# Kernel optimization log

Measured on AMD Instinct MI355X. Metric: run time of the kernel, lower is better.

## Reference

```python
import jax, jax.numpy as jnp
import numpy as np

B, S, D, E = 4, 2048, 1024, 8
HD = D // E          # per-expert head dim = 128
ROPE = HD // 2       # rotary dims = 64 (32 complex pairs)


def setup_inputs() -> dict:
    key = jax.random.key(0)
    ks = jax.random.split(key, 5)
    x = jax.random.normal(ks[0], (B, S, D), dtype=jnp.float32)
    Wg = jax.random.normal(ks[1], (D, E), dtype=jnp.float32) * 0.02
    Wqkv = jax.random.normal(ks[2], (E, D, 3 * HD), dtype=jnp.float32) * 0.02
    Wff = jax.random.normal(ks[3], (E, HD, D), dtype=jnp.float32) * 0.02
    b_ff = jnp.zeros((D,), dtype=jnp.float32)
    # precompute_freqs_cis(qk_rope_head_dim=ROPE, seqlen=S), theta=10000
    inv = 1.0 / (10000.0 ** (np.arange(0, ROPE, 2, dtype=np.float32) / ROPE))  # [ROPE//2]
    ang = np.arange(S, dtype=np.float32)[:, None] * inv[None, :]               # [S, ROPE//2]
    cos = jnp.asarray(np.cos(ang), dtype=jnp.float32)
    sin = jnp.asarray(np.sin(ang), dtype=jnp.float32)
    return {"x": x, "Wg": Wg, "Wqkv": Wqkv, "Wff": Wff, "b_ff": b_ff, "cos": cos, "sin": sin}


def _apply_rope(x, cos, sin):
    # x: [B,S,E,HD]; rotate the second half (x_pe), keep first half (x_nope), cat (pe, nope)
    b, s, e, hd = x.shape
    x_nope, x_pe = x[..., : hd // 2], x[..., hd // 2 :]
    xr = x_pe.reshape(b, s, e, hd // 4, 2)
    re, im = xr[..., 0], xr[..., 1]
    c = cos[None, :, None, :]
    sn = sin[None, :, None, :]
    rot = jnp.stack([re * c - im * sn, re * sn + im * c], axis=-1).reshape(b, s, e, hd // 2)
    return jnp.concatenate([rot, x_nope], axis=-1)


def reference(x, Wg, Wqkv, Wff, b_ff, cos, sin):
    b, s, d = x.shape
    e, hd = Wqkv.shape[0], Wqkv.shape[2] // 3
    # RoPE on per-expert chunks
    xh = _apply_rope(x.reshape(b, s, e, hd), cos, sin).reshape(b, s, d)
    # SwitchGate: top-1 routing
    probs = jax.nn.softmax(xh @ Wg, axis=-1)            # [b,s,E]
    expert = jnp.argmax(probs, axis=-1)                 # [b,s]
    gate = jnp.max(probs, axis=-1)                      # [b,s]
    # preprocess: per-expert stable gather of routed tokens (capacity = s, padded+masked)
    is_e = expert[None, :, :] == jnp.arange(e)[:, None, None]        # [E,b,s] bool
    order = jnp.argsort(jnp.where(is_e, 0, 1), axis=-1, stable=True)  # [E,b,s] routed-first
    mask_g = jnp.take_along_axis(is_e, order, axis=-1).astype(xh.dtype)  # [E,b,s]
    x_g = jnp.take_along_axis(xh[None], order[..., None], axis=2)    # [E,b,s,d]
    gate_g = jnp.take_along_axis(gate[None], order, axis=2)          # [E,b,s]
    # expert-grouped column-parallel QKV
    qkv = jnp.einsum("ebsd,edf->ebsf", x_g, Wqkv)                    # [E,b,s,3*hd]
    q, k, v = jnp.split(qkv, 3, axis=-1)                             # [E,b,s,hd]
    # grouped sparse attention within each expert's token set
    dot = jnp.einsum("ebqh,ebkh->ebqk", q, k) / jnp.sqrt(jnp.asarray(hd, xh.dtype))
    dot = dot - 1e6 * (1.0 - mask_g[:, :, None, :])
    attn = jax.nn.softmax(dot, axis=-1)
    ctx = jnp.einsum("ebqk,ebkh->ebqh", attn, v)                     # [E,b,s,hd]
    # row-parallel output projection, gate-weighted
    out = jnp.einsum("ebsh,ehd->ebsd", ctx, Wff) + b_ff
    out = out * (gate_g * mask_g)[..., None]
    # scatter_add combine back to [b,s,d]
    outs = jnp.zeros((b, s, d), dtype=xh.dtype)
    outs = outs.at[jnp.arange(b)[None, :, None], order].add(out)
    return outs
```

## Files before the change

kernel.cpp:

```cpp
#include <hip/hip_runtime.h>
#include <math.h>

#define Bn 4
#define Sn 2048
#define Dn 1024
#define En 8
#define HDn 128
#define NG 32
#define MAXT 160
#define MAXN 1024

typedef __attribute__((ext_vector_type(8))) short bf16x8;
typedef __attribute__((ext_vector_type(4))) float f32x4;
typedef unsigned short u16;

__device__ __forceinline__ unsigned bf16_rn(float x) {
  unsigned u = __float_as_uint(x);
  return (u + 0x7fffu + ((u >> 16) & 1u)) >> 16;
}
__device__ __forceinline__ void bsplit(float x, unsigned& hi, unsigned& lo) {
  hi = bf16_rn(x);
  lo = bf16_rn(x - __uint_as_float(hi << 16));
}
__device__ __forceinline__ void gl16(const void* g, void* l) {
  __builtin_amdgcn_global_load_lds(
      (const __attribute__((address_space(1))) void*)g,
      (__attribute__((address_space(3))) void*)l, 16, 0, 0);
}
#define MFMA16(a, b, c) __builtin_amdgcn_mfma_f32_16x16x32_bf16((a), (b), (c), 0, 0, 0)

__global__ __launch_bounds__(256) void k_rope_gate(
    const float* __restrict__ x, const float* __restrict__ Wg,
    const float* __restrict__ cosT, const float* __restrict__ sinT,
    u16* __restrict__ xh_hi, u16* __restrict__ xh_lo,
    int* __restrict__ expertArr, float* __restrict__ gateArr)
{
  int wid = threadIdx.x >> 6, l = threadIdx.x & 63;
  int bs = (blockIdx.x << 2) + wid;
  int s  = bs & (Sn - 1);
  const float* xrow = x + (size_t)bs * Dn;
  int j0 = l << 4;
  int hb = j0 & ~127;
  int jj = j0 & 127;
  float v[16];
  if (jj < 64) {
    const float* pe = xrow + hb + 64 + jj;
    float a[16];
    *(float4*)(a + 0)  = *(const float4*)(pe + 0);
    *(float4*)(a + 4)  = *(const float4*)(pe + 4);
    *(float4*)(a + 8)  = *(const float4*)(pe + 8);
    *(float4*)(a + 12) = *(const float4*)(pe + 12);
    int p0 = jj >> 1;
#pragma unroll
    for (int i = 0; i < 8; ++i) {
      float c  = cosT[s * 32 + p0 + i];
      float sn = sinT[s * 32 + p0 + i];
      v[2 * i]     = a[2 * i] * c - a[2 * i + 1] * sn;
      v[2 * i + 1] = a[2 * i] * sn + a[2 * i + 1] * c;
    }
  } else {
    const float* np = xrow + hb + (jj - 64);
    *(float4*)(v + 0)  = *(const float4*)(np + 0);
    *(float4*)(v + 4)  = *(const float4*)(np + 4);
    *(float4*)(v + 8)  = *(const float4*)(np + 8);
    *(float4*)(v + 12) = *(const float4*)(np + 12);
  }
  u16 hh[16] __attribute__((aligned(16)));
  u16 ll[16] __attribute__((aligned(16)));
#pragma unroll
  for (int i = 0; i < 16; ++i) {
    unsigned h, lo;
    bsplit(v[i], h, lo);
    hh[i] = (u16)h; ll[i] = (u16)lo;
  }
  *(uint4*)(xh_hi + (size_t)bs * Dn + j0)     = *(uint4*)(hh);
  *(uint4*)(xh_hi + (size_t)bs * Dn + j0 + 8) = *(uint4*)(hh + 8);
  *(uint4*)(xh_lo + (size_t)bs * Dn + j0)     = *(uint4*)(ll);
  *(uint4*)(xh_lo + (size_t)bs * Dn + j0 + 8) = *(uint4*)(ll + 8);

  float pl[8] = {0.f, 0.f, 0.f, 0.f, 0.f, 0.f, 0.f, 0.f};
  const float* wr = Wg + (size_t)j0 * En;
#pragma unroll
  for (int i = 0; i < 16; ++i) {
    float4 w0 = *(const float4*)(wr + i * 8);
    float4 w1 = *(const float4*)(wr + i * 8 + 4);
    float xv = v[i];
    pl[0] += xv * w0.x; pl[1] += xv * w0.y; pl[2] += xv * w0.z; pl[3] += xv * w0.w;
    pl[4] += xv * w1.x; pl[5] += xv * w1.y; pl[6] += xv * w1.z; pl[7] += xv * w1.w;
  }
#pragma unroll
  for (int off = 1; off < 64; off <<= 1) {
#pragma unroll
    for (int e = 0; e < 8; ++e) pl[e] += __shfl_xor(pl[e], off, 64);
  }
  float m = pl[0]; int be = 0;
#pragma unroll
  for (int e = 1; e < 8; ++e) if (pl[e] > m) { m = pl[e]; be = e; }
  float ss = 0.f;
#pragma unroll
  for (int e = 0; e < 8; ++e) ss += expf(pl[e] - m);
  if (l == 0) {
    expertArr[bs] = be;
    gateArr[bs] = 1.0f / ss;
  }
}

__global__ __launch_bounds__(256) void k_prep_w(
    const float* __restrict__ W, u16* __restrict__ hiT, u16* __restrict__ loT,
    int Kdim, int Ndim)
{
  int e = blockIdx.z, k0 = blockIdx.x << 6, c0 = blockIdx.y << 6;
  __shared__ float tile[64][65];
  int t = threadIdx.x;
  int r = t >> 4, cc = (t & 15) << 2;
  const float* src = W + ((size_t)e * Kdim + k0) * Ndim + c0;
#pragma unroll
  for (int i = 0; i < 4; ++i) {
    float4 v = *(const float4*)(src + (size_t)(r + i * 16) * Ndim + cc);
    tile[r + i * 16][cc + 0] = v.x; tile[r + i * 16][cc + 1] = v.y;
    tile[r + i * 16][cc + 2] = v.z; tile[r + i * 16][cc + 3] = v.w;
  }
  __syncthreads();
#pragma unroll
  for (int i = 0; i < 4; ++i) {
    int oc = (t >> 4) + i * 16;
    int ok = (t & 15) << 2;
    float v0 = tile[ok + 0][oc], v1 = tile[ok + 1][oc];
    float v2 = tile[ok + 2][oc], v3 = tile[ok + 3][oc];
    unsigned h0,l0,h1,l1,h2,l2,h3,l3;
    bsplit(v0,h0,l0); bsplit(v1,h1,l1); bsplit(v2,h2,l2); bsplit(v3,h3,l3);
    size_t o = ((size_t)e * Ndim + c0 + oc) * Kdim + k0 + ok;
    *(ushort4*)(hiT + o) = make_ushort4((u16)h0,(u16)h1,(u16)h2,(u16)h3);
    *(ushort4*)(loT + o) = make_ushort4((u16)l0,(u16)l1,(u16)l2,(u16)l3);
  }
}

__global__ __launch_bounds__(256) void k_route(
    const int* __restrict__ expertArr, int* __restrict__ idx, int* __restrict__ cnt)
{
  int g = blockIdx.x;
  int b = g >> 3, e = g & 7;
  int t = threadIdx.x;
  __shared__ int wtot[4];
  __shared__ int base;
  if (t == 0) base = 0;
  __syncthreads();
  for (int c = 0; c < Sn; c += 256) {
    int s = c + t;
    int pred = (expertArr[b * Sn + s] == e) ? 1 : 0;
    unsigned long long mask = __ballot(pred);
    int ln = t & 63, wv = t >> 6;
    int wpre = __popcll(mask & ((1ull << ln) - 1ull));
    if (ln == 63) wtot[wv] = wpre + pred;
    __syncthreads();
    int woff = 0;
    for (int w = 0; w < wv; ++w) woff += wtot[w];
    int tot = wtot[0] + wtot[1] + wtot[2] + wtot[3];
    if (pred) idx[(g << 11) + base + woff + wpre] = s;
    __syncthreads();
    if (t == 0) base += tot;
    __syncthreads();
  }
  if (t == 0) cnt[g] = base;
}

__global__ void k_tiles(const int* __restrict__ cnt, int* __restrict__ tileg,
                        int* __restrict__ tilem, int* __restrict__ ntile)
{
  if (threadIdx.x == 0 && blockIdx.x == 0) {
    int t = 0;
    for (int g = 0; g < NG; ++g) {
      int n = cnt[g];
      for (int m0 = 0; m0 < n && t < MAXT; m0 += 64) { tileg[t] = g; tilem[t] = m0; ++t; }
    }
    ntile[0] = t;
  }
}

__global__ __launch_bounds__(256) void k_qkv(
    const u16* __restrict__ xh_hi, const u16* __restrict__ xh_lo,
    const u16* __restrict__ WqT_hi, const u16* __restrict__ WqT_lo,
    const int* __restrict__ idx, const int* __restrict__ cnt,
    u16* __restrict__ qkv_hi, u16* __restrict__ qkv_lo,
    u16* __restrict__ vT_hi, u16* __restrict__ vT_lo)
{
  extern __shared__ unsigned char LDS[];
  int bid = blockIdx.x;
  int r8 = bid & 7, q = bid >> 3;
  int g = r8 + ((q & 3) << 3);
  int slot = q >> 2;
  int m0 = (slot >> 1) << 6;
  int n0 = (slot & 1) * 192;
  int n = cnt[g];
  if (m0 >= n) return;
  int b = g >> 3, e = g & 7;
  const int* idxg = idx + (g << 11);
  int t = threadIdx.x;
  int w = t >> 6, l = t & 63;
  int lc = l & 15, lq = l >> 4;

  int srow = t >> 2;
  int sslot = (t & 3) ^ ((srow >> 1) & 3);
  int rgs = m0 + srow; rgs = rgs < n ? rgs : n - 1;
  size_t aoffR = ((size_t)(b * Sn + idxg[rgs])) * Dn + sslot * 8;
  size_t boffR0 = ((size_t)e * 384 + n0 + srow) * Dn + sslot * 8;
  unsigned dst = (unsigned)t << 4;

  f32x4 acc[4][3];
#pragma unroll
  for (int i = 0; i < 4; ++i)
#pragma unroll
    for (int j = 0; j < 3; ++j) acc[i][j] = (f32x4){0.f, 0.f, 0.f, 0.f};

  unsigned off = (unsigned)((lq ^ ((lc >> 1) & 3)) << 4);

#define STAGE(bb, k0)                                                 \
  do {                                                                \
    gl16(xh_hi + aoffR + (k0), LDS + (bb) + dst);                     \
    gl16(xh_lo + aoffR + (k0), LDS + (bb) + 4096 + dst);              \
    gl16(WqT_hi + boffR0 + (k0), LDS + (bb) + 8192 + dst);            \
    gl16(WqT_hi + boffR0 + (size_t)64 * Dn + (k0), LDS + (bb) + 12288 + dst); \
    gl16(WqT_hi + boffR0 + (size_t)128 * Dn + (k0), LDS + (bb) + 16384 + dst);\
    gl16(WqT_lo + boffR0 + (k0), LDS + (bb) + 20480 + dst);           \
    gl16(WqT_lo + boffR0 + (size_t)64 * Dn + (k0), LDS + (bb) + 24576 + dst); \
    gl16(WqT_lo + boffR0 + (size_t)128 * Dn + (k0), LDS + (bb) + 28672 + dst);\
  } while (0)

  STAGE(0, 0);
  __syncthreads();
  for (int tt = 0; tt < 32; ++tt) {
    unsigned cur = (tt & 1) ? 32768u : 0u;
    if (tt < 31) STAGE(cur ^ 32768u, (tt + 1) * 32);
    bf16x8 ah[4], al[4], bh[3], bl[3];
#pragma unroll
    for (int fi = 0; fi < 4; ++fi) {
      unsigned ab = cur + (unsigned)((fi * 16 + lc) * 64) + off;
      ah[fi] = *(const bf16x8*)(LDS + ab);
      al[fi] = *(const bf16x8*)(LDS + ab + 4096);
    }
#pragma unroll
    for (int fj = 0; fj < 3; ++fj) {
      unsigned bb2 = cur + 8192u + (unsigned)((w * 48 + fj * 16 + lc) * 64) + off;
      bh[fj] = *(const bf16x8*)(LDS + bb2);
      bl[fj] = *(const bf16x8*)(LDS + bb2 + 12288);
    }
#pragma unroll
    for (int fi = 0; fi < 4; ++fi)
#pragma unroll
      for (int fj = 0; fj < 3; ++fj) {
        acc[fi][fj] = MFMA16(ah[fi], bh[fj], acc[fi][fj]);
        acc[fi][fj] = MFMA16(al[fi], bh[fj], acc[fi][fj]);
        acc[fi][fj] = MFMA16(ah[fi], bl[fj], acc[fi][fj]);
      }
    __syncthreads();
  }
#undef STAGE

#pragma unroll
  for (int fi = 0; fi < 4; ++fi) {
#pragma unroll
    for (int rr = 0; rr < 4; ++rr) {
      int rg = m0 + fi * 16 + lq * 4 + rr;
      if (rg < n) {
        int tok = idxg[rg];
#pragma unroll
        for (int fj = 0; fj < 3; ++fj) {
          int col = n0 + w * 48 + fj * 16 + lc;
          unsigned h, lo2;
          bsplit(acc[fi][fj][rr], h, lo2);
          if (col < 256) {
            size_t o = (size_t)(b * Sn + tok) * 384 + col;
            qkv_hi[o] = (u16)h; qkv_lo[o] = (u16)lo2;
          } else {
            size_t o = ((size_t)g * HDn + (col - 256)) * MAXN + rg;
            vT_hi[o] = (u16)h; vT_lo[o] = (u16)lo2;
          }
        }
      }
    }
  }
}

__global__ __launch_bounds__(256) void k_attn(
    const u16* __restrict__ qkv_hi, const u16* __restrict__ qkv_lo,
    const u16* __restrict__ vT_hi, const u16* __restrict__ vT_lo,
    const int* __restrict__ idx, const int* __restrict__ cnt,
    const int* __restrict__ tileg, const int* __restrict__ tilem,
    const int* __restrict__ ntile,
    u16* __restrict__ ctx_hi, u16* __restrict__ ctx_lo)
{
  extern __shared__ unsigned char LDS[];
  int tid = blockIdx.x;
  if (tid >= ntile[0]) return;
  int g = tileg[tid], m0 = tilem[tid];
  int n = cnt[g];
  int b = g >> 3;
  const int* idxg = idx + (g << 11);
  int t = threadIdx.x, wid = t >> 6, l = t & 63;
  int lc = l & 15, lq = l >> 4;
  const float scale = 0.08838834764831845f;

  int qrg = m0 + wid * 16 + lc; qrg = qrg < n ? qrg : n - 1;
  size_t qoff = (size_t)(b * Sn + idxg[qrg]) * 384 + lq * 8;
  bf16x8 Qhi[4], Qlo[4];
#pragma unroll
  for (int ks = 0; ks < 4; ++ks) {
    Qhi[ks] = *(const bf16x8*)(qkv_hi + qoff + ks * 32);
    Qlo[ks] = *(const bf16x8*)(qkv_lo + qoff + ks * 32);
  }

  f32x4 acc[8];
#pragma unroll
  for (int i = 0; i < 8; ++i) acc[i] = (f32x4){0.f, 0.f, 0.f, 0.f};
  float m_r[4] = {-1e30f, -1e30f, -1e30f, -1e30f};
  float l_r[4] = {0.f, 0.f, 0.f, 0.f};

  size_t vbase = ((size_t)g * HDn + lc) * MAXN + lq * 8;
  unsigned pbase = 65536u + wid * 4096u;

#define STAGEK(bufb, kc)                                                     \
  do {                                                                       \
    unsigned bb = (bufb);                                                    \
    for (int j = 0; j < 4; ++j) {                                            \
      int c = wid * 4 + j;                                                   \
      int row = (kc) + c * 4 + lq;                                           \
      int rg = row < n ? row : n - 1;                                        \
      int srcslot = lc ^ (((c & 1) << 2) | lq);                              \
      size_t soff = (size_t)(b * Sn + idxg[rg]) * 384 + 128 + srcslot * 8;   \
      gl16(qkv_hi + soff, LDS + bb + c * 1024);                              \
      gl16(qkv_lo + soff, LDS + bb + 16384 + c * 1024);                      \
    }                                                                        \
  } while (0)

  int nt = (n + 63) >> 6;
  STAGEK(0, 0);
  __syncthreads();

  for (int tt = 0; tt < nt; ++tt) {
    unsigned cur = (tt & 1) ? 32768u : 0u;
    if (tt + 1 < nt) STAGEK(cur ^ 32768u, (tt + 1) * 64);
    int kc = tt * 64;

    f32x4 Sf[4];
#pragma unroll
    for (int kf = 0; kf < 4; ++kf) Sf[kf] = (f32x4){0.f, 0.f, 0.f, 0.f};
#pragma unroll
    for (int ks = 0; ks < 4; ++ks) {
#pragma unroll
      for (int kf = 0; kf < 4; ++kf) {
        int row = kf * 16 + lc;
        unsigned byte = cur + row * 256 + ((((ks << 2) | lq) ^ (row & 7)) << 4);
        bf16x8 kh = *(const bf16x8*)(LDS + byte);
        bf16x8 kl = *(const bf16x8*)(LDS + byte + 16384);
        Sf[kf] = MFMA16(Qhi[ks], kh, Sf[kf]);
        Sf[kf] = MFMA16(Qlo[ks], kh, Sf[kf]);
        Sf[kf] = MFMA16(Qhi[ks], kl, Sf[kf]);
      }
    }

    float mloc[4] = {-1e30f, -1e30f, -1e30f, -1e30f};
#pragma unroll
    for (int kf = 0; kf < 4; ++kf) {
#pragma unroll
      for (int r = 0; r < 4; ++r) {
        int key = kc + kf * 16 + lc;
        float s = (key < n) ? Sf[kf][r] * scale : -1e30f;
        Sf[kf][r] = s;
        mloc[r] = fmaxf(mloc[r], s);
      }
    }
#pragma unroll
    for (int off = 1; off < 16; off <<= 1) {
#pragma unroll
      for (int r = 0; r < 4; ++r) mloc[r] = fmaxf(mloc[r], __shfl_xor(mloc[r], off, 64));
    }
    float corr[4], rs[4] = {0.f, 0.f, 0.f, 0.f};
#pragma unroll
    for (int r = 0; r < 4; ++r) {
      float mn = fmaxf(m_r[r], mloc[r]);
      corr[r] = expf(m_r[r] - mn);
      m_r[r] = mn;
    }
#pragma unroll
    for (int kf = 0; kf < 4; ++kf) {
#pragma unroll
      for (int r = 0; r < 4; ++r) {
        float p = expf(Sf[kf][r] - m_r[r]);
        rs[r] += p;
        unsigned ph, plo;
        bsplit(p, ph, plo);
        int prow = (lq << 2) | r;
        int slot = (kf << 1) | (lc >> 3);
        unsigned pb = pbase + prow * 128 + ((slot ^ (prow & 7)) << 4) + ((lc & 7) << 1);
        *(u16*)(LDS + pb) = (u16)ph;
        *(u16*)(LDS + pb + 2048) = (u16)plo;
      }
    }
#pragma unroll
    for (int off = 1; off < 16; off <<= 1) {
#pragma unroll
      for (int r = 0; r < 4; ++r) rs[r] += __shfl_xor(rs[r], off, 64);
    }
#pragma unroll
    for (int r = 0; r < 4; ++r) l_r[r] = l_r[r] * corr[r] + rs[r];
#pragma unroll
    for (int df = 0; df < 8; ++df)
#pragma unroll
      for (int r = 0; r < 4; ++r) acc[df][r] *= corr[r];

#pragma unroll
    for (int ks2 = 0; ks2 < 2; ++ks2) {
      unsigned pr = pbase + lc * 128 + ((((ks2 << 2) | lq) ^ (lc & 7)) << 4);
      bf16x8 pa = *(const bf16x8*)(LDS + pr);
      bf16x8 pl = *(const bf16x8*)(LDS + pr + 2048);
#pragma unroll
      for (int df = 0; df < 8; ++df) {
        size_t vo = vbase + (size_t)(df * 16) * MAXN + kc + ks2 * 32;
        bf16x8 vh = *(const bf16x8*)(vT_hi + vo);
        bf16x8 vl = *(const bf16x8*)(vT_lo + vo);
        acc[df] = MFMA16(pa, vh, acc[df]);
        acc[df] = MFMA16(pl, vh, acc[df]);
        acc[df] = MFMA16(pa, vl, acc[df]);
      }
    }
    __syncthreads();
  }
#undef STAGEK

#pragma unroll
  for (int r = 0; r < 4; ++r) {
    int rg = m0 + wid * 16 + (lq << 2) + r;
    if (rg < n) {
      int tok = idxg[rg];
      float inv = 1.0f / l_r[r];
      size_t o = (size_t)(b * Sn + tok) * HDn + lc;
#pragma unroll
      for (int df = 0; df < 8; ++df) {
        unsigned h, lo2;
        bsplit(acc[df][r] * inv, h, lo2);
        ctx_hi[o + df * 16] = (u16)h;
        ctx_lo[o + df * 16] = (u16)lo2;
      }
    }
  }
}

__global__ __launch_bounds__(256) void k_out(
    const u16* __restrict__ ctx_hi, const u16* __restrict__ ctx_lo,
    const u16* __restrict__ WfT_hi, const u16* __restrict__ WfT_lo,
    const float* __restrict__ bff,
    const int* __restrict__ idx, const int* __restrict__ cnt,
    const int* __restrict__ tileg, const int* __restrict__ tilem,
    const int* __restrict__ ntile,
    const float* __restrict__ gateArr,
    float* __restrict__ out)
{
  int tid = blockIdx.x;
  if (tid >= ntile[0]) return;
  int g = tileg[tid], m0 = tilem[tid];
  int n = cnt[g];
  int b = g >> 3, e = g & 7;
  const int* idxg = idx + (g << 11);
  int t = threadIdx.x, wid = t >> 6, l = t & 63;
  int lc = l & 15, lq = l >> 4;
  int n0 = blockIdx.y * 256 + wid * 64;

  f32x4 acc[4][4];
#pragma unroll
  for (int i = 0; i < 4; ++i)
#pragma unroll
    for (int j = 0; j < 4; ++j) acc[i][j] = (f32x4){0.f, 0.f, 0.f, 0.f};

  size_t aoff[4];
#pragma unroll
  for (int fi = 0; fi < 4; ++fi) {
    int rg = m0 + fi * 16 + lc; rg = rg < n ? rg : n - 1;
    aoff[fi] = ((size_t)(b * Sn + idxg[rg])) * HDn + lq * 8;
  }
  size_t boff[4];
#pragma unroll
  for (int fj = 0; fj < 4; ++fj)
    boff[fj] = ((size_t)e * Dn + n0 + fj * 16 + lc) * HDn + lq * 8;

#pragma unroll
  for (int ks = 0; ks < 4; ++ks) {
    int ko = ks * 32;
    bf16x8 ah[4], al[4], bh[4], bl[4];
#pragma unroll
    for (int fi = 0; fi < 4; ++fi) {
      ah[fi] = *(const bf16x8*)(ctx_hi + aoff[fi] + ko);
      al[fi] = *(const bf16x8*)(ctx_lo + aoff[fi] + ko);
    }
#pragma unroll
    for (int fj = 0; fj < 4; ++fj) {
      bh[fj] = *(const bf16x8*)(WfT_hi + boff[fj] + ko);
      bl[fj] = *(const bf16x8*)(WfT_lo + boff[fj] + ko);
    }
#pragma unroll
    for (int fi = 0; fi < 4; ++fi)
#pragma unroll
      for (int fj = 0; fj < 4; ++fj) {
        acc[fi][fj] = MFMA16(ah[fi], bh[fj], acc[fi][fj]);
        acc[fi][fj] = MFMA16(al[fi], bh[fj], acc[fi][fj]);
        acc[fi][fj] = MFMA16(ah[fi], bl[fj], acc[fi][fj]);
      }
  }

  float bv[4];
#pragma unroll
  for (int fj = 0; fj < 4; ++fj) bv[fj] = bff[n0 + fj * 16 + lc];

#pragma unroll
  for (int fi = 0; fi < 4; ++fi) {
#pragma unroll
    for (int rr = 0; rr < 4; ++rr) {
      int rg = m0 + fi * 16 + lq * 4 + rr;
      if (rg < n) {
        int tok = idxg[rg];
        float gt = gateArr[b * Sn + tok];
        float* orow = out + ((size_t)(b * Sn + tok)) * Dn + n0 + lc;
#pragma unroll
        for (int fj = 0; fj < 4; ++fj)
          orow[fj * 16] = (acc[fi][fj][rr] + bv[fj]) * gt;
      }
    }
  }
}

extern "C" void kernel_launch(void* const* d_in, const int* in_sizes, int n_in,
                              void* d_out, int out_size, void* d_ws, size_t ws_size,
                              hipStream_t stream) {
  const float* x    = (const float*)d_in[0];
  const float* Wg   = (const float*)d_in[1];
  const float* Wqkv = (const float*)d_in[2];
  const float* Wff  = (const float*)d_in[3];
  const float* bff  = (const float*)d_in[4];
  const float* cosT = (const float*)d_in[5];
  const float* sinT = (const float*)d_in[6];
  float* out = (float*)d_out;

  size_t off = 0;
  auto carve = [&](size_t bytes) -> void* {
    void* p = (char*)d_ws + off;
    off += (bytes + 255) & ~(size_t)255;
    return p;
  };
  u16* xh_hi  = (u16*)carve((size_t)Bn * Sn * Dn * 2);
  u16* xh_lo  = (u16*)carve((size_t)Bn * Sn * Dn * 2);
  u16* WqT_hi = (u16*)carve((size_t)En * 384 * Dn * 2);
  u16* WqT_lo = (u16*)carve((size_t)En * 384 * Dn * 2);
  u16* WfT_hi = (u16*)carve((size_t)En * Dn * HDn * 2);
  u16* WfT_lo = (u16*)carve((size_t)En * Dn * HDn * 2);
  u16* qkv_hi = (u16*)carve((size_t)Bn * Sn * 384 * 2);
  u16* qkv_lo = (u16*)carve((size_t)Bn * Sn * 384 * 2);
  u16* vT_hi  = (u16*)carve((size_t)NG * HDn * MAXN * 2);
  u16* vT_lo  = (u16*)carve((size_t)NG * HDn * MAXN * 2);
  u16* ctx_hi = (u16*)carve((size_t)Bn * Sn * HDn * 2);
  u16* ctx_lo = (u16*)carve((size_t)Bn * Sn * HDn * 2);
  float* gateArr = (float*)carve((size_t)Bn * Sn * sizeof(float));
  int*   expertA = (int*)carve((size_t)Bn * Sn * sizeof(int));
  int*   idx     = (int*)carve((size_t)NG * Sn * sizeof(int));
  int*   cnt     = (int*)carve((size_t)NG * sizeof(int));
  int*   tileg   = (int*)carve((size_t)MAXT * sizeof(int));
  int*   tilem   = (int*)carve((size_t)MAXT * sizeof(int));
  int*   ntile   = (int*)carve(256);
  (void)ws_size; (void)in_sizes; (void)n_in; (void)out_size;

  hipFuncSetAttribute((const void*)k_attn, hipFuncAttributeMaxDynamicSharedMemorySize, 81920);

  k_rope_gate<<<dim3(Bn * Sn / 4), dim3(256), 0, stream>>>(x, Wg, cosT, sinT, xh_hi, xh_lo, expertA, gateArr);
  k_prep_w<<<dim3(16, 6, 8), dim3(256), 0, stream>>>(Wqkv, WqT_hi, WqT_lo, Dn, 384);
  k_prep_w<<<dim3(2, 16, 8), dim3(256), 0, stream>>>(Wff, WfT_hi, WfT_lo, HDn, Dn);
  k_route<<<dim3(NG), dim3(256), 0, stream>>>(expertA, idx, cnt);
  k_tiles<<<dim3(1), dim3(64), 0, stream>>>(cnt, tileg, tilem, ntile);
  k_qkv<<<dim3(384), dim3(256), 65536, stream>>>(xh_hi, xh_lo, WqT_hi, WqT_lo, idx, cnt, qkv_hi, qkv_lo, vT_hi, vT_lo);
  k_attn<<<dim3(MAXT), dim3(256), 81920, stream>>>(qkv_hi, qkv_lo, vT_hi, vT_lo, idx, cnt, tileg, tilem, ntile, ctx_hi, ctx_lo);
  k_out<<<dim3(MAXT, 4), dim3(256), 0, stream>>>(ctx_hi, ctx_lo, WfT_hi, WfT_lo, bff, idx, cnt, tileg, tilem, ntile, gateArr, out);
}
```

Before: 191.2 us.

## Merge prologue kernels, fold tile building into route, loosen qkv pipeline waits

Merges rope/gate and both weight-prep launches into one prologue kernel that dispatches work by block index. The separate tile-list kernel is removed: the last route block to finish, detected with an atomic counter, builds the tile list. This cuts three launches and their gaps. The qkv main loop also replaces __syncthreads with explicit vmcnt/lgkmcnt waits and raw barriers, so the next stage's global loads can stay in flight while MFMAs run. The risks are the counter reset and memory-ordering correctness, plus the hand-picked wait count depending on the load count per stage.

```diff
diff --git a/kernel.cpp b/kernel.cpp
--- a/kernel.cpp
+++ b/kernel.cpp
@@ -29,88 +29,10 @@
 }
 #define MFMA16(a, b, c) __builtin_amdgcn_mfma_f32_16x16x32_bf16((a), (b), (c), 0, 0, 0)
 
-__global__ __launch_bounds__(256) void k_rope_gate(
-    const float* __restrict__ x, const float* __restrict__ Wg,
-    const float* __restrict__ cosT, const float* __restrict__ sinT,
-    u16* __restrict__ xh_hi, u16* __restrict__ xh_lo,
-    int* __restrict__ expertArr, float* __restrict__ gateArr)
+__device__ __forceinline__ void prep_body(
+    const float* __restrict__ W, u16* __restrict__ hiT, u16* __restrict__ loT,
+    int Kdim, int Ndim, int e, int k0, int c0, float (*tile)[65])
 {
-  int wid = threadIdx.x >> 6, l = threadIdx.x & 63;
-  int bs = (blockIdx.x << 2) + wid;
-  int s  = bs & (Sn - 1);
-  const float* xrow = x + (size_t)bs * Dn;
-  int j0 = l << 4;
-  int hb = j0 & ~127;
-  int jj = j0 & 127;
-  float v[16];
-  if (jj < 64) {
-    const float* pe = xrow + hb + 64 + jj;
-    float a[16];
-    *(float4*)(a + 0)  = *(const float4*)(pe + 0);
-    *(float4*)(a + 4)  = *(const float4*)(pe + 4);
-    *(float4*)(a + 8)  = *(const float4*)(pe + 8);
-    *(float4*)(a + 12) = *(const float4*)(pe + 12);
-    int p0 = jj >> 1;
-#pragma unroll
-    for (int i = 0; i < 8; ++i) {
-      float c  = cosT[s * 32 + p0 + i];
-      float sn = sinT[s * 32 + p0 + i];
-      v[2 * i]     = a[2 * i] * c - a[2 * i + 1] * sn;
-      v[2 * i + 1] = a[2 * i] * sn + a[2 * i + 1] * c;
-    }
-  } else {
-    const float* np = xrow + hb + (jj - 64);
-    *(float4*)(v + 0)  = *(const float4*)(np + 0);
-    *(float4*)(v + 4)  = *(const float4*)(np + 4);
-    *(float4*)(v + 8)  = *(const float4*)(np + 8);
-    *(float4*)(v + 12) = *(const float4*)(np + 12);
-  }
-  u16 hh[16] __attribute__((aligned(16)));
-  u16 ll[16] __attribute__((aligned(16)));
-#pragma unroll
-  for (int i = 0; i < 16; ++i) {
-    unsigned h, lo;
-    bsplit(v[i], h, lo);
-    hh[i] = (u16)h; ll[i] = (u16)lo;
-  }
-  *(uint4*)(xh_hi + (size_t)bs * Dn + j0)     = *(uint4*)(hh);
-  *(uint4*)(xh_hi + (size_t)bs * Dn + j0 + 8) = *(uint4*)(hh + 8);
-  *(uint4*)(xh_lo + (size_t)bs * Dn + j0)     = *(uint4*)(ll);
-  *(uint4*)(xh_lo + (size_t)bs * Dn + j0 + 8) = *(uint4*)(ll + 8);
-
-  float pl[8] = {0.f, 0.f, 0.f, 0.f, 0.f, 0.f, 0.f, 0.f};
-  const float* wr = Wg + (size_t)j0 * En;
-#pragma unroll
-  for (int i = 0; i < 16; ++i) {
-    float4 w0 = *(const float4*)(wr + i * 8);
-    float4 w1 = *(const float4*)(wr + i * 8 + 4);
-    float xv = v[i];
-    pl[0] += xv * w0.x; pl[1] += xv * w0.y; pl[2] += xv * w0.z; pl[3] += xv * w0.w;
-    pl[4] += xv * w1.x; pl[5] += xv * w1.y; pl[6] += xv * w1.z; pl[7] += xv * w1.w;
-  }
-#pragma unroll
-  for (int off = 1; off < 64; off <<= 1) {
-#pragma unroll
-    for (int e = 0; e < 8; ++e) pl[e] += __shfl_xor(pl[e], off, 64);
-  }
-  float m = pl[0]; int be = 0;
-#pragma unroll
-  for (int e = 1; e < 8; ++e) if (pl[e] > m) { m = pl[e]; be = e; }
-  float ss = 0.f;
-#pragma unroll
-  for (int e = 0; e < 8; ++e) ss += expf(pl[e] - m);
-  if (l == 0) {
-    expertArr[bs] = be;
-    gateArr[bs] = 1.0f / ss;
-  }
-}
-
-__global__ __launch_bounds__(256) void k_prep_w(
-    const float* __restrict__ W, u16* __restrict__ hiT, u16* __restrict__ loT,
-    int Kdim, int Ndim)
-{
-  int e = blockIdx.z, k0 = blockIdx.x << 6, c0 = blockIdx.y << 6;
-  __shared__ float tile[64][65];
   int t = threadIdx.x;
   int r = t >> 4, cc = (t & 15) << 2;
   const float* src = W + ((size_t)e * Kdim + k0) * Ndim + c0;
@@ -135,8 +57,103 @@
   }
 }
 
+__global__ __launch_bounds__(256) void k_prologue(
+    const float* __restrict__ x, const float* __restrict__ Wg,
+    const float* __restrict__ cosT, const float* __restrict__ sinT,
+    const float* __restrict__ Wqkv, const float* __restrict__ Wff,
+    u16* __restrict__ xh_hi, u16* __restrict__ xh_lo,
+    u16* __restrict__ WqT_hi, u16* __restrict__ WqT_lo,
+    u16* __restrict__ WfT_hi, u16* __restrict__ WfT_lo,
+    int* __restrict__ expertArr, float* __restrict__ gateArr,
+    int* __restrict__ done)
+{
+  __shared__ float tile[64][65];
+  int bid = blockIdx.x;
+  if (bid == 0 && threadIdx.x == 0) done[0] = 0;
+  if (bid < 2048) {
+    int wid = threadIdx.x >> 6, l = threadIdx.x & 63;
+    int bs = (bid << 2) + wid;
+    int s  = bs & (Sn - 1);
+    const float* xrow = x + (size_t)bs * Dn;
+    int j0 = l << 4;
+    int hb = j0 & ~127;
+    int jj = j0 & 127;
+    float v[16];
+    if (jj < 64) {
+      const float* pe = xrow + hb + 64 + jj;
+      float a[16];
+      *(float4*)(a + 0)  = *(const float4*)(pe + 0);
+      *(float4*)(a + 4)  = *(const float4*)(pe + 4);
+      *(float4*)(a + 8)  = *(const float4*)(pe + 8);
+      *(float4*)(a + 12) = *(const float4*)(pe + 12);
+      int p0 = jj >> 1;
+#pragma unroll
+      for (int i = 0; i < 8; ++i) {
+        float c  = cosT[s * 32 + p0 + i];
+        float sn = sinT[s * 32 + p0 + i];
+        v[2 * i]     = a[2 * i] * c - a[2 * i + 1] * sn;
+        v[2 * i + 1] = a[2 * i] * sn + a[2 * i + 1] * c;
+      }
+    } else {
+      const float* np = xrow + hb + (jj - 64);
+      *(float4*)(v + 0)  = *(const float4*)(np + 0);
+      *(float4*)(v + 4)  = *(const float4*)(np + 4);
+      *(float4*)(v + 8)  = *(const float4*)(np + 8);
+      *(float4*)(v + 12) = *(const float4*)(np + 12);
+    }
+    u16 hh[16] __attribute__((aligned(16)));
+    u16 ll[16] __attribute__((aligned(16)));
+#pragma unroll
+    for (int i = 0; i < 16; ++i) {
+      unsigned h, lo;
+      bsplit(v[i], h, lo);
+      hh[i] = (u16)h; ll[i] = (u16)lo;
+    }
+    *(uint4*)(xh_hi + (size_t)bs * Dn + j0)     = *(uint4*)(hh);
+    *(uint4*)(xh_hi + (size_t)bs * Dn + j0 + 8) = *(uint4*)(hh + 8);
+    *(uint4*)(xh_lo + (size_t)bs * Dn + j0)     = *(uint4*)(ll);
+    *(uint4*)(xh_lo + (size_t)bs * Dn + j0 + 8) = *(uint4*)(ll + 8);
+
+    float pl[8] = {0.f, 0.f, 0.f, 0.f, 0.f, 0.f, 0.f, 0.f};
+    const float* wr = Wg + (size_t)j0 * En;
+#pragma unroll
+    for (int i = 0; i < 16; ++i) {
+      float4 w0 = *(const float4*)(wr + i * 8);
+      float4 w1 = *(const float4*)(wr + i * 8 + 4);
+      float xv = v[i];
+      pl[0] += xv * w0.x; pl[1] += xv * w0.y; pl[2] += xv * w0.z; pl[3] += xv * w0.w;
+      pl[4] += xv * w1.x; pl[5] += xv * w1.y; pl[6] += xv * w1.z; pl[7] += xv * w1.w;
+    }
+#pragma unroll
+    for (int off = 1; off < 64; off <<= 1) {
+#pragma unroll
+      for (int e = 0; e < 8; ++e) pl[e] += __shfl_xor(pl[e], off, 64);
+    }
+    float m = pl[0]; int be = 0;
+#pragma unroll
+    for (int e = 1; e < 8; ++e) if (pl[e] > m) { m = pl[e]; be = e; }
+    float ss = 0.f;
+#pragma unroll
+    for (int e = 0; e < 8; ++e) ss += expf(pl[e] - m);
+    if (l == 0) {
+      expertArr[bs] = be;
+      gateArr[bs] = 1.0f / ss;
+    }
+  } else if (bid < 2048 + 768) {
+    int id = bid - 2048;
+    int e = id / 96, r2 = id % 96;
+    prep_body(Wqkv, WqT_hi, WqT_lo, Dn, 384, e, (r2 / 6) << 6, (r2 % 6) << 6, tile);
+  } else {
+    int id = bid - 2816;
+    int e = id >> 5, r2 = id & 31;
+    prep_body(Wff, WfT_hi, WfT_lo, HDn, Dn, e, (r2 >> 4) << 6, (r2 & 15) << 6, tile);
+  }
+}
+
 __global__ __launch_bounds__(256) void k_route(
-    const int* __restrict__ expertArr, int* __restrict__ idx, int* __restrict__ cnt)
+    const int* __restrict__ expertArr, int* __restrict__ idx, int* __restrict__ cnt,
+    int* __restrict__ tileg, int* __restrict__ tilem, int* __restrict__ ntile,
+    int* __restrict__ done)
 {
   int g = blockIdx.x;
   int b = g >> 3, e = g & 7;
@@ -161,19 +178,17 @@
     if (t == 0) base += tot;
     __syncthreads();
   }
-  if (t == 0) cnt[g] = base;
-}
-
-__global__ void k_tiles(const int* __restrict__ cnt, int* __restrict__ tileg,
-                        int* __restrict__ tilem, int* __restrict__ ntile)
-{
-  if (threadIdx.x == 0 && blockIdx.x == 0) {
-    int t = 0;
-    for (int g = 0; g < NG; ++g) {
-      int n = cnt[g];
-      for (int m0 = 0; m0 < n && t < MAXT; m0 += 64) { tileg[t] = g; tilem[t] = m0; ++t; }
-    }
-    ntile[0] = t;
+  if (t == 0) {
+    cnt[g] = base;
+    __threadfence();
+    if (atomicAdd(done, 1) == NG - 1) {
+      int tc = 0;
+      for (int gg = 0; gg < NG; ++gg) {
+        int nn = __hip_atomic_load(&cnt[gg], __ATOMIC_ACQUIRE, __HIP_MEMORY_SCOPE_AGENT);
+        for (int m0 = 0; m0 < nn && tc < MAXT; m0 += 64) { tileg[tc] = gg; tilem[tc] = m0; ++tc; }
+      }
+      ntile[0] = tc;
+    }
   }
 }
 
@@ -227,10 +242,17 @@
   } while (0)
 
   STAGE(0, 0);
-  __syncthreads();
+  asm volatile("s_waitcnt vmcnt(0)" ::: "memory");
+  __builtin_amdgcn_s_barrier();
   for (int tt = 0; tt < 32; ++tt) {
     unsigned cur = (tt & 1) ? 32768u : 0u;
-    if (tt < 31) STAGE(cur ^ 32768u, (tt + 1) * 32);
+    if (tt < 31) {
+      STAGE(cur ^ 32768u, (tt + 1) * 32);
+      asm volatile("s_waitcnt vmcnt(8)" ::: "memory");
+    } else {
+      asm volatile("s_waitcnt vmcnt(0)" ::: "memory");
+    }
+    __builtin_amdgcn_s_barrier();
     bf16x8 ah[4], al[4], bh[3], bl[3];
 #pragma unroll
     for (int fi = 0; fi < 4; ++fi) {
@@ -252,7 +274,9 @@
         acc[fi][fj] = MFMA16(al[fi], bh[fj], acc[fi][fj]);
         acc[fi][fj] = MFMA16(ah[fi], bl[fj], acc[fi][fj]);
       }
-    __syncthreads();
+    asm volatile("s_waitcnt lgkmcnt(0)" ::: "memory");
+    __builtin_amdgcn_sched_barrier(0);
+    __builtin_amdgcn_s_barrier();
   }
 #undef STAGE
 
@@ -564,15 +588,14 @@
   int*   tileg   = (int*)carve((size_t)MAXT * sizeof(int));
   int*   tilem   = (int*)carve((size_t)MAXT * sizeof(int));
   int*   ntile   = (int*)carve(256);
+  int*   done    = (int*)carve(256);
   (void)ws_size; (void)in_sizes; (void)n_in; (void)out_size;
 
   hipFuncSetAttribute((const void*)k_attn, hipFuncAttributeMaxDynamicSharedMemorySize, 81920);
 
-  k_rope_gate<<<dim3(Bn * Sn / 4), dim3(256), 0, stream>>>(x, Wg, cosT, sinT, xh_hi, xh_lo, expertA, gateArr);
-  k_prep_w<<<dim3(16, 6, 8), dim3(256), 0, stream>>>(Wqkv, WqT_hi, WqT_lo, Dn, 384);
-  k_prep_w<<<dim3(2, 16, 8), dim3(256), 0, stream>>>(Wff, WfT_hi, WfT_lo, HDn, Dn);
-  k_route<<<dim3(NG), dim3(256), 0, stream>>>(expertA, idx, cnt);
-  k_tiles<<<dim3(1), dim3(64), 0, stream>>>(cnt, tileg, tilem, ntile);
+  k_prologue<<<dim3(3072), dim3(256), 0, stream>>>(x, Wg, cosT, sinT, Wqkv, Wff,
+      xh_hi, xh_lo, WqT_hi, WqT_lo, WfT_hi, WfT_lo, expertA, gateArr, done);
+  k_route<<<dim3(NG), dim3(256), 0, stream>>>(expertA, idx, cnt, tileg, tilem, ntile, done);
   k_qkv<<<dim3(384), dim3(256), 65536, stream>>>(xh_hi, xh_lo, WqT_hi, WqT_lo, idx, cnt, qkv_hi, qkv_lo, vT_hi, vT_lo);
   k_attn<<<dim3(MAXT), dim3(256), 81920, stream>>>(qkv_hi, qkv_lo, vT_hi, vT_lo, idx, cnt, tileg, tilem, ntile, ctx_hi, ctx_lo);
   k_out<<<dim3(MAXT, 4), dim3(256), 0, stream>>>(ctx_hi, ctx_lo, WfT_hi, WfT_lo, bff, idx, cnt, tileg, tilem, ntile, gateArr, out);
```

Measured after the change: 186.9 us. -2.3%, faster.
